# Kernel optimization log

Measured on AMD Instinct MI355X. Metric: run time of the kernel, lower is better.

## Reference

```python
import jax, jax.numpy as jnp
import numpy as np

IN_FEATS = 512
OUT_FEATS = 512


def _xavier(key, shape, gain):
    fan_in, fan_out = shape[1], shape[0]
    a = gain * np.sqrt(6.0 / (fan_in + fan_out))
    return jax.random.uniform(key, shape, jnp.float32, -a, a)


def setup_inputs() -> dict:
    key = jax.random.key(0)
    ks = jax.random.split(key, 8)
    num_dst, num_vir, num_src = 8192, 32768, 131072
    n_e0, n_e1 = 524288, 131072
    gain = np.sqrt(2.0)  # calculate_gain('relu')
    feat = jax.random.normal(ks[0], (num_dst + num_src, IN_FEATS), jnp.float32)
    W_self = _xavier(ks[1], (OUT_FEATS, IN_FEATS), gain)
    b_self = jnp.zeros((OUT_FEATS,), jnp.float32)
    W_neigh = _xavier(ks[2], (OUT_FEATS, IN_FEATS), gain)
    e0_src = jax.random.randint(ks[3], (n_e0,), 0, num_src, jnp.int64 if jax.config.jax_enable_x64 else jnp.int32)
    e0_dst = jax.random.randint(ks[4], (n_e0,), 0, num_vir, e0_src.dtype)
    e1_src = jax.random.randint(ks[5], (n_e1,), 0, num_vir, e0_src.dtype)
    e1_dst = jax.random.randint(ks[6], (n_e1,), 0, num_dst, e0_src.dtype)
    return {
        "feat": feat, "W_self": W_self, "b_self": b_self, "W_neigh": W_neigh,
        "e0_src": e0_src, "e0_dst": e0_dst, "e1_src": e1_src, "e1_dst": e1_dst,
        "num_dst": num_dst, "num_vir": num_vir,
    }


def _seg_mean(msgs, dst, n):
    # DGL fn.mean: mean over incoming edges; zero-in-degree nodes get 0.
    s = jax.ops.segment_sum(msgs, dst, num_segments=n)
    c = jax.ops.segment_sum(jnp.ones((dst.shape[0], 1), msgs.dtype), dst, num_segments=n)
    return s / jnp.maximum(c, 1.0)


def reference(feat, W_self, b_self, W_neigh, e0_src, e0_dst, e1_src, e1_dst, num_dst, num_vir):
    # feat_drop is identity (p=0.0)
    h_dst = feat[:num_dst] @ W_self.T + b_self              # [num_dst, out]
    feat_src = feat[num_dst:]                                # [num_src, in]
    h_src = feat_src @ W_neigh.T                             # [num_src, out]
    # block0: copy_u + mean -> virtual nodes
    h_vir = _seg_mean(h_src[e0_src], e0_dst, num_vir)        # [num_vir, out]
    # SPFeatureShuffle is identity in single-partition setting
    # block1: copy_u + mean -> dst nodes
    h_neigh = _seg_mean(h_vir[e1_src], e1_dst, num_dst)      # [num_dst, out]
    rst = h_dst + h_neigh                                    # activation=None, norm=None
    return rst
```

## Files before the change

### kernel.cpp

```cpp
#include <hip/hip_runtime.h>
#include <stdint.h>

#define NUM_DST 8192
#define NUM_VIR 32768
#define NUM_SRC 131072
#define F       512
#define CAP     64

typedef short bf16x8 __attribute__((ext_vector_type(8)));
typedef float f32x4  __attribute__((ext_vector_type(4)));
typedef float f32x2  __attribute__((ext_vector_type(2)));
typedef unsigned int u32x4 __attribute__((ext_vector_type(4)));

__device__ __forceinline__ unsigned short f2bf(float f) {
  union { float f; unsigned int u; } v; v.f = f;
  unsigned int u = v.u;
  unsigned int r = (u + 0x7fffu + ((u >> 16) & 1u)) >> 16;
  return (unsigned short)r;
}
__device__ __forceinline__ unsigned int pack2(float a, float b) {
  return (unsigned int)f2bf(a) | ((unsigned int)f2bf(b) << 16);
}

__global__ void prep_all(const int* __restrict__ e0s, const int* __restrict__ e0d, int ne0,
                         const int* __restrict__ e1s, const int* __restrict__ e1d, int ne1,
                         int* __restrict__ c0, int* __restrict__ b0,
                         int* __restrict__ c1, int* __restrict__ b1,
                         const float* __restrict__ feat,
                         const float* __restrict__ Wself, const float* __restrict__ Wneigh,
                         u32x4* __restrict__ a1, u32x4* __restrict__ fsrc8,
                         unsigned short* __restrict__ wcat,
                         int bktBlocks, int a1Blocks, int srcBlocks) {
  int b = blockIdx.x, t = threadIdx.x;
  if (b < bktBlocks) {
    int i = b * 256 + t;
    if (i < ne0) {
      int d = e0d[i];
      int r = atomicAdd(&c0[d], 1);
      if (r < CAP) b0[d * CAP + r] = e0s[i];
    } else {
      int j = i - ne0;
      if (j < ne1) {
        int d = e1d[j];
        int r = atomicAdd(&c1[d], 1);
        if (r < CAP) b1[d * CAP + r] = e1s[j];
      }
    }
  } else if (b < bktBlocks + a1Blocks) {
    size_t tid = (size_t)(b - bktBlocks) * 256 + t;
    const f32x4* fp = (const f32x4*)feat;
    f32x4 v0 = __builtin_nontemporal_load(&fp[tid * 2]);
    f32x4 v1 = __builtin_nontemporal_load(&fp[tid * 2 + 1]);
    u32x4 o;
    o.x = pack2(v0.x, v0.y); o.y = pack2(v0.z, v0.w);
    o.z = pack2(v1.x, v1.y); o.w = pack2(v1.z, v1.w);
    a1[tid] = o;
  } else if (b < bktBlocks + a1Blocks + srcBlocks) {
    size_t idx = (size_t)(b - bktBlocks - a1Blocks) * 256 + t;
    const f32x4* fp = (const f32x4*)(feat + (size_t)NUM_DST * F);
    f32x4 v0 = __builtin_nontemporal_load(&fp[idx * 4]);
    f32x4 v1 = __builtin_nontemporal_load(&fp[idx * 4 + 1]);
    f32x4 v2 = __builtin_nontemporal_load(&fp[idx * 4 + 2]);
    f32x4 v3 = __builtin_nontemporal_load(&fp[idx * 4 + 3]);
    u32x4 o;
    o.x = __builtin_amdgcn_cvt_pk_fp8_f32(v0.x, v0.y, 0u, 0);
    o.x = __builtin_amdgcn_cvt_pk_fp8_f32(v0.z, v0.w, o.x, 1);
    o.y = __builtin_amdgcn_cvt_pk_fp8_f32(v1.x, v1.y, 0u, 0);
    o.y = __builtin_amdgcn_cvt_pk_fp8_f32(v1.z, v1.w, o.y, 1);
    o.z = __builtin_amdgcn_cvt_pk_fp8_f32(v2.x, v2.y, 0u, 0);
    o.z = __builtin_amdgcn_cvt_pk_fp8_f32(v2.z, v2.w, o.z, 1);
    o.w = __builtin_amdgcn_cvt_pk_fp8_f32(v3.x, v3.y, 0u, 0);
    o.w = __builtin_amdgcn_cvt_pk_fp8_f32(v3.z, v3.w, o.w, 1);
    fsrc8[idx] = o;
  } else {
    int idx = (b - bktBlocks - a1Blocks - srcBlocks) * 256 + t;
    int n = idx >> 7, kb = (idx & 127) * 8;
    const float* src = (kb < F) ? (Wself + (size_t)n * F + kb)
                                : (Wneigh + (size_t)n * F + (kb - F));
    f32x4 v0 = __builtin_nontemporal_load((const f32x4*)src);
    f32x4 v1 = __builtin_nontemporal_load((const f32x4*)(src + 4));
    u32x4 o;
    o.x = pack2(v0.x, v0.y); o.y = pack2(v0.z, v0.w);
    o.z = pack2(v1.x, v1.y); o.w = pack2(v1.z, v1.w);
    *(u32x4*)(wcat + (size_t)n * 1024 + kb) = o;
  }
}

template<bool OUT_FP8>
__global__ void agg_gather(const uint4* __restrict__ tab, const int* __restrict__ cnt,
                           const int* __restrict__ bucket, void* __restrict__ outp) {
  int seg  = blockIdx.x * 4 + (threadIdx.x >> 6);
  int lane = threadIdx.x & 63;
  int half = lane >> 5;
  int l32  = lane & 31;
  int c = cnt[seg]; if (c > CAP) c = CAP;
  const int* bk = bucket + (size_t)seg * CAP;
  float a[16];
#pragma unroll
  for (int j = 0; j < 16; ++j) a[j] = 0.f;
  for (int i = half; i < c; i += 2) {
    int s = bk[i];
    uint4 u = tab[(size_t)s * 32 + l32];
    f32x2 p;
    p = __builtin_amdgcn_cvt_pk_f32_fp8(u.x, 0); a[0]  += p.x; a[1]  += p.y;
    p = __builtin_amdgcn_cvt_pk_f32_fp8(u.x, 1); a[2]  += p.x; a[3]  += p.y;
    p = __builtin_amdgcn_cvt_pk_f32_fp8(u.y, 0); a[4]  += p.x; a[5]  += p.y;
    p = __builtin_amdgcn_cvt_pk_f32_fp8(u.y, 1); a[6]  += p.x; a[7]  += p.y;
    p = __builtin_amdgcn_cvt_pk_f32_fp8(u.z, 0); a[8]  += p.x; a[9]  += p.y;
    p = __builtin_amdgcn_cvt_pk_f32_fp8(u.z, 1); a[10] += p.x; a[11] += p.y;
    p = __builtin_amdgcn_cvt_pk_f32_fp8(u.w, 0); a[12] += p.x; a[13] += p.y;
    p = __builtin_amdgcn_cvt_pk_f32_fp8(u.w, 1); a[14] += p.x; a[15] += p.y;
  }
#pragma unroll
  for (int j = 0; j < 16; ++j) a[j] += __shfl_xor(a[j], 32);
  float inv = 1.0f / (float)(c < 1 ? 1 : c);
  if (half == 0) {
    if (OUT_FP8) {
      uint4 o;
      o.x = __builtin_amdgcn_cvt_pk_fp8_f32(a[0] * inv,  a[1] * inv,  0u, 0);
      o.x = __builtin_amdgcn_cvt_pk_fp8_f32(a[2] * inv,  a[3] * inv,  o.x, 1);
      o.y = __builtin_amdgcn_cvt_pk_fp8_f32(a[4] * inv,  a[5] * inv,  0u, 0);
      o.y = __builtin_amdgcn_cvt_pk_fp8_f32(a[6] * inv,  a[7] * inv,  o.y, 1);
      o.z = __builtin_amdgcn_cvt_pk_fp8_f32(a[8] * inv,  a[9] * inv,  0u, 0);
      o.z = __builtin_amdgcn_cvt_pk_fp8_f32(a[10] * inv, a[11] * inv, o.z, 1);
      o.w = __builtin_amdgcn_cvt_pk_fp8_f32(a[12] * inv, a[13] * inv, 0u, 0);
      o.w = __builtin_amdgcn_cvt_pk_fp8_f32(a[14] * inv, a[15] * inv, o.w, 1);
      ((uint4*)outp)[(size_t)seg * 32 + l32] = o;
    } else {
      uint4 o0, o1;
      o0.x = pack2(a[0] * inv,  a[1] * inv);  o0.y = pack2(a[2] * inv,  a[3] * inv);
      o0.z = pack2(a[4] * inv,  a[5] * inv);  o0.w = pack2(a[6] * inv,  a[7] * inv);
      o1.x = pack2(a[8] * inv,  a[9] * inv);  o1.y = pack2(a[10] * inv, a[11] * inv);
      o1.z = pack2(a[12] * inv, a[13] * inv); o1.w = pack2(a[14] * inv, a[15] * inv);
      uint4* orow = (uint4*)outp + (size_t)seg * 64 + l32 * 2;
      orow[0] = o0;
      orow[1] = o1;
    }
  }
}

__global__ __launch_bounds__(256) void gemm_kernel(
    const unsigned short* __restrict__ A1, const unsigned short* __restrict__ A2,
    const unsigned short* __restrict__ W, const float* __restrict__ bias,
    float* __restrict__ out) {
  __shared__ unsigned short As[128 * 72];
  __shared__ unsigned short Bs[64 * 72];
  int t = threadIdx.x;
  int lane = t & 63, wid = t >> 6;
  int wm = wid & 1, wn = wid >> 1;
  int l16 = lane & 15, quad = lane >> 4;
  int m0 = blockIdx.x * 128, n0 = blockIdx.y * 64;

  f32x4 acc[4][2];
  for (int fi = 0; fi < 4; ++fi)
    for (int ni = 0; ni < 2; ++ni)
      acc[fi][ni] = (f32x4){0.f, 0.f, 0.f, 0.f};

  for (int kt = 0; kt < 16; ++kt) {
    const unsigned short* Asrc = (kt < 8) ? A1 : A2;
    int kk0 = (kt & 7) * 64;
#pragma unroll
    for (int r = 0; r < 4; ++r) {
      int q = r * 256 + t;
      int row = q >> 3, c = q & 7;
      uint4 v = *(const uint4*)(Asrc + (size_t)(m0 + row) * F + kk0 + c * 8);
      *(uint4*)(&As[row * 72 + c * 8]) = v;
    }
#pragma unroll
    for (int r = 0; r < 2; ++r) {
      int q = r * 256 + t;
      int row = q >> 3, c = q & 7;
      uint4 v = *(const uint4*)(W + (size_t)(n0 + row) * 1024 + kt * 64 + c * 8);
      *(uint4*)(&Bs[row * 72 + c * 8]) = v;
    }
    __syncthreads();
#pragma unroll
    for (int kk = 0; kk < 2; ++kk) {
      bf16x8 a[4], b[2];
#pragma unroll
      for (int fi = 0; fi < 4; ++fi)
        a[fi] = *(const bf16x8*)(&As[(wm * 64 + fi * 16 + l16) * 72 + kk * 32 + quad * 8]);
#pragma unroll
      for (int ni = 0; ni < 2; ++ni)
        b[ni] = *(const bf16x8*)(&Bs[(wn * 32 + ni * 16 + l16) * 72 + kk * 32 + quad * 8]);
#pragma unroll
      for (int fi = 0; fi < 4; ++fi)
#pragma unroll
        for (int ni = 0; ni < 2; ++ni)
          acc[fi][ni] = __builtin_amdgcn_mfma_f32_16x16x32_bf16(a[fi], b[ni], acc[fi][ni], 0, 0, 0);
    }
    __syncthreads();
  }
#pragma unroll
  for (int ni = 0; ni < 2; ++ni) {
    int n = n0 + wn * 32 + ni * 16 + l16;
    float bv = bias[n];
#pragma unroll
    for (int fi = 0; fi < 4; ++fi) {
#pragma unroll
      for (int reg = 0; reg < 4; ++reg) {
        int m = m0 + wm * 64 + fi * 16 + quad * 4 + reg;
        __builtin_nontemporal_store(acc[fi][ni][reg] + bv, &out[(size_t)m * F + n]);
      }
    }
  }
}

extern "C" void kernel_launch(void* const* d_in, const int* in_sizes, int n_in,
                              void* d_out, int out_size, void* d_ws, size_t ws_size,
                              hipStream_t stream) {
  const float* feat    = (const float*)d_in[0];
  const float* W_self  = (const float*)d_in[1];
  const float* b_self  = (const float*)d_in[2];
  const float* W_neigh = (const float*)d_in[3];
  const int*   e0_src  = (const int*)d_in[4];
  const int*   e0_dst  = (const int*)d_in[5];
  const int*   e1_src  = (const int*)d_in[6];
  const int*   e1_dst  = (const int*)d_in[7];
  int ne0 = in_sizes[4];
  int ne1 = in_sizes[6];

  char* ws = (char*)d_ws;
  size_t off = 0;
  auto nxt = [&](size_t bytes) -> char* {
    char* p = ws + off;
    off += (bytes + 255) & ~(size_t)255;
    return p;
  };
  int* cnt0    = (int*)nxt((size_t)NUM_VIR * 4);
  int* cnt1    = (int*)nxt((size_t)NUM_DST * 4);
  int* bucket0 = (int*)nxt((size_t)NUM_VIR * CAP * 4);
  int* bucket1 = (int*)nxt((size_t)NUM_DST * CAP * 4);
  u32x4* fsrc8 = (u32x4*)nxt((size_t)NUM_SRC * F);
  u32x4* a1    = (u32x4*)nxt((size_t)NUM_DST * F * 2);
  uint2* fvir8 = (uint2*)nxt((size_t)NUM_VIR * F);
  uint4* a2    = (uint4*)nxt((size_t)NUM_DST * F * 2);
  unsigned short* wcat = (unsigned short*)nxt((size_t)F * 1024 * 2);
  (void)ws_size;

  hipMemsetAsync(cnt0, 0, (size_t)(NUM_VIR + NUM_DST) * 4, stream);

  int neTot     = ne0 + ne1;
  int bktBlocks = (neTot + 255) / 256;
  int a1Blocks  = NUM_DST * F / 8 / 256;
  int srcBlocks = NUM_SRC * F / 16 / 256;
  prep_all<<<bktBlocks + a1Blocks + srcBlocks + 256, 256, 0, stream>>>(
      e0_src, e0_dst, ne0, e1_src, e1_dst, ne1,
      cnt0, bucket0, cnt1, bucket1,
      feat, W_self, W_neigh, a1, fsrc8, wcat,
      bktBlocks, a1Blocks, srcBlocks);

  agg_gather<true><<<NUM_VIR / 4, 256, 0, stream>>>((const uint4*)fsrc8, cnt0, bucket0, fvir8);
  agg_gather<false><<<NUM_DST / 4, 256, 0, stream>>>((const uint4*)fvir8, cnt1, bucket1, a2);

  dim3 ggrid(NUM_DST / 128, F / 64);
  gemm_kernel<<<ggrid, 256, 0, stream>>>((const unsigned short*)a1, (const unsigned short*)a2,
                                         wcat, b_self, (float*)d_out);
}
```

Baseline: 520.9 us.

## Gather four edge rows per wave in aggregation and XOR-swizzle GEMM LDS tiles

```diff
diff --git a/kernel.cpp b/kernel.cpp
--- a/kernel.cpp
+++ b/kernel.cpp
@@ -91,50 +91,85 @@
                            const int* __restrict__ bucket, void* __restrict__ outp) {
   int seg  = blockIdx.x * 4 + (threadIdx.x >> 6);
   int lane = threadIdx.x & 63;
-  int half = lane >> 5;
-  int l32  = lane & 31;
+  int q    = lane >> 4;
+  int l16  = lane & 15;
   int c = cnt[seg]; if (c > CAP) c = CAP;
   const int* bk = bucket + (size_t)seg * CAP;
-  float a[16];
-#pragma unroll
-  for (int j = 0; j < 16; ++j) a[j] = 0.f;
-  for (int i = half; i < c; i += 2) {
-    int s = bk[i];
-    uint4 u = tab[(size_t)s * 32 + l32];
+  int myidx = bk[lane];
+  const uint4* lanebase = tab + l16 * 2;
+  float a[32];
+#pragma unroll
+  for (int j = 0; j < 32; ++j) a[j] = 0.f;
+  int nit = (c + 3) >> 2;
+  for (int k = 0; k < nit; ++k) {
+    int i = k * 4 + q;
+    bool ok = i < c;
+    int s = __shfl(myidx, i);
+    uint4 u0 = make_uint4(0u, 0u, 0u, 0u);
+    uint4 u1 = make_uint4(0u, 0u, 0u, 0u);
+    if (ok) {
+      const uint4* rp = lanebase + (size_t)s * 32;
+      u0 = rp[0];
+      u1 = rp[1];
+    }
     f32x2 p;
-    p = __builtin_amdgcn_cvt_pk_f32_fp8(u.x, 0); a[0]  += p.x; a[1]  += p.y;
-    p = __builtin_amdgcn_cvt_pk_f32_fp8(u.x, 1); a[2]  += p.x; a[3]  += p.y;
-    p = __builtin_amdgcn_cvt_pk_f32_fp8(u.y, 0); a[4]  += p.x; a[5]  += p.y;
-    p = __builtin_amdgcn_cvt_pk_f32_fp8(u.y, 1); a[6]  += p.x; a[7]  += p.y;
-    p = __builtin_amdgcn_cvt_pk_f32_fp8(u.z, 0); a[8]  += p.x; a[9]  += p.y;
-    p = __builtin_amdgcn_cvt_pk_f32_fp8(u.z, 1); a[10] += p.x; a[11] += p.y;
-    p = __builtin_amdgcn_cvt_pk_f32_fp8(u.w, 0); a[12] += p.x; a[13] += p.y;
-    p = __builtin_amdgcn_cvt_pk_f32_fp8(u.w, 1); a[14] += p.x; a[15] += p.y;
-  }
-#pragma unroll
-  for (int j = 0; j < 16; ++j) a[j] += __shfl_xor(a[j], 32);
+    p = __builtin_amdgcn_cvt_pk_f32_fp8(u0.x, 0); a[0]  += p.x; a[1]  += p.y;
+    p = __builtin_amdgcn_cvt_pk_f32_fp8(u0.x, 1); a[2]  += p.x; a[3]  += p.y;
+    p = __builtin_amdgcn_cvt_pk_f32_fp8(u0.y, 0); a[4]  += p.x; a[5]  += p.y;
+    p = __builtin_amdgcn_cvt_pk_f32_fp8(u0.y, 1); a[6]  += p.x; a[7]  += p.y;
+    p = __builtin_amdgcn_cvt_pk_f32_fp8(u0.z, 0); a[8]  += p.x; a[9]  += p.y;
+    p = __builtin_amdgcn_cvt_pk_f32_fp8(u0.z, 1); a[10] += p.x; a[11] += p.y;
+    p = __builtin_amdgcn_cvt_pk_f32_fp8(u0.w, 0); a[12] += p.x; a[13] += p.y;
+    p = __builtin_amdgcn_cvt_pk_f32_fp8(u0.w, 1); a[14] += p.x; a[15] += p.y;
+    p = __builtin_amdgcn_cvt_pk_f32_fp8(u1.x, 0); a[16] += p.x; a[17] += p.y;
+    p = __builtin_amdgcn_cvt_pk_f32_fp8(u1.x, 1); a[18] += p.x; a[19] += p.y;
+    p = __builtin_amdgcn_cvt_pk_f32_fp8(u1.y, 0); a[20] += p.x; a[21] += p.y;
+    p = __builtin_amdgcn_cvt_pk_f32_fp8(u1.y, 1); a[22] += p.x; a[23] += p.y;
+    p = __builtin_amdgcn_cvt_pk_f32_fp8(u1.z, 0); a[24] += p.x; a[25] += p.y;
+    p = __builtin_amdgcn_cvt_pk_f32_fp8(u1.z, 1); a[26] += p.x; a[27] += p.y;
+    p = __builtin_amdgcn_cvt_pk_f32_fp8(u1.w, 0); a[28] += p.x; a[29] += p.y;
+    p = __builtin_amdgcn_cvt_pk_f32_fp8(u1.w, 1); a[30] += p.x; a[31] += p.y;
+  }
+#pragma unroll
+  for (int j = 0; j < 32; ++j) {
+    a[j] += __shfl_xor(a[j], 16);
+    a[j] += __shfl_xor(a[j], 32);
+  }
   float inv = 1.0f / (float)(c < 1 ? 1 : c);
-  if (half == 0) {
+  if (q == 0) {
     if (OUT_FP8) {
-      uint4 o;
-      o.x = __builtin_amdgcn_cvt_pk_fp8_f32(a[0] * inv,  a[1] * inv,  0u, 0);
-      o.x = __builtin_amdgcn_cvt_pk_fp8_f32(a[2] * inv,  a[3] * inv,  o.x, 1);
-      o.y = __builtin_amdgcn_cvt_pk_fp8_f32(a[4] * inv,  a[5] * inv,  0u, 0);
-      o.y = __builtin_amdgcn_cvt_pk_fp8_f32(a[6] * inv,  a[7] * inv,  o.y, 1);
-      o.z = __builtin_amdgcn_cvt_pk_fp8_f32(a[8] * inv,  a[9] * inv,  0u, 0);
-      o.z = __builtin_amdgcn_cvt_pk_fp8_f32(a[10] * inv, a[11] * inv, o.z, 1);
-      o.w = __builtin_amdgcn_cvt_pk_fp8_f32(a[12] * inv, a[13] * inv, 0u, 0);
-      o.w = __builtin_amdgcn_cvt_pk_fp8_f32(a[14] * inv, a[15] * inv, o.w, 1);
-      ((uint4*)outp)[(size_t)seg * 32 + l32] = o;
+      uint4 o0, o1;
+      o0.x = __builtin_amdgcn_cvt_pk_fp8_f32(a[0] * inv,  a[1] * inv,  0u, 0);
+      o0.x = __builtin_amdgcn_cvt_pk_fp8_f32(a[2] * inv,  a[3] * inv,  o0.x, 1);
+      o0.y = __builtin_amdgcn_cvt_pk_fp8_f32(a[4] * inv,  a[5] * inv,  0u, 0);
+      o0.y = __builtin_amdgcn_cvt_pk_fp8_f32(a[6] * inv,  a[7] * inv,  o0.y, 1);
+      o0.z = __builtin_amdgcn_cvt_pk_fp8_f32(a[8] * inv,  a[9] * inv,  0u, 0);
+      o0.z = __builtin_amdgcn_cvt_pk_fp8_f32(a[10] * inv, a[11] * inv, o0.z, 1);
+      o0.w = __builtin_amdgcn_cvt_pk_fp8_f32(a[12] * inv, a[13] * inv, 0u, 0);
+      o0.w = __builtin_amdgcn_cvt_pk_fp8_f32(a[14] * inv, a[15] * inv, o0.w, 1);
+      o1.x = __builtin_amdgcn_cvt_pk_fp8_f32(a[16] * inv, a[17] * inv, 0u, 0);
+      o1.x = __builtin_amdgcn_cvt_pk_fp8_f32(a[18] * inv, a[19] * inv, o1.x, 1);
+      o1.y = __builtin_amdgcn_cvt_pk_fp8_f32(a[20] * inv, a[21] * inv, 0u, 0);
+      o1.y = __builtin_amdgcn_cvt_pk_fp8_f32(a[22] * inv, a[23] * inv, o1.y, 1);
+      o1.z = __builtin_amdgcn_cvt_pk_fp8_f32(a[24] * inv, a[25] * inv, 0u, 0);
+      o1.z = __builtin_amdgcn_cvt_pk_fp8_f32(a[26] * inv, a[27] * inv, o1.z, 1);
+      o1.w = __builtin_amdgcn_cvt_pk_fp8_f32(a[28] * inv, a[29] * inv, 0u, 0);
+      o1.w = __builtin_amdgcn_cvt_pk_fp8_f32(a[30] * inv, a[31] * inv, o1.w, 1);
+      uint4* op = (uint4*)outp + (size_t)seg * 32 + l16 * 2;
+      op[0] = o0;
+      op[1] = o1;
     } else {
-      uint4 o0, o1;
-      o0.x = pack2(a[0] * inv,  a[1] * inv);  o0.y = pack2(a[2] * inv,  a[3] * inv);
-      o0.z = pack2(a[4] * inv,  a[5] * inv);  o0.w = pack2(a[6] * inv,  a[7] * inv);
-      o1.x = pack2(a[8] * inv,  a[9] * inv);  o1.y = pack2(a[10] * inv, a[11] * inv);
+      uint4 o0, o1, o2, o3;
+      o0.x = pack2(a[0]  * inv, a[1]  * inv); o0.y = pack2(a[2]  * inv, a[3]  * inv);
+      o0.z = pack2(a[4]  * inv, a[5]  * inv); o0.w = pack2(a[6]  * inv, a[7]  * inv);
+      o1.x = pack2(a[8]  * inv, a[9]  * inv); o1.y = pack2(a[10] * inv, a[11] * inv);
       o1.z = pack2(a[12] * inv, a[13] * inv); o1.w = pack2(a[14] * inv, a[15] * inv);
-      uint4* orow = (uint4*)outp + (size_t)seg * 64 + l32 * 2;
-      orow[0] = o0;
-      orow[1] = o1;
+      o2.x = pack2(a[16] * inv, a[17] * inv); o2.y = pack2(a[18] * inv, a[19] * inv);
+      o2.z = pack2(a[20] * inv, a[21] * inv); o2.w = pack2(a[22] * inv, a[23] * inv);
+      o3.x = pack2(a[24] * inv, a[25] * inv); o3.y = pack2(a[26] * inv, a[27] * inv);
+      o3.z = pack2(a[28] * inv, a[29] * inv); o3.w = pack2(a[30] * inv, a[31] * inv);
+      uint4* op = (uint4*)outp + (size_t)seg * 64 + l16 * 4;
+      op[0] = o0; op[1] = o1; op[2] = o2; op[3] = o3;
     }
   }
 }
@@ -143,8 +178,8 @@
     const unsigned short* __restrict__ A1, const unsigned short* __restrict__ A2,
     const unsigned short* __restrict__ W, const float* __restrict__ bias,
     float* __restrict__ out) {
-  __shared__ unsigned short As[128 * 72];
-  __shared__ unsigned short Bs[64 * 72];
+  __shared__ unsigned short As[128 * 64];
+  __shared__ unsigned short Bs[64 * 64];
   int t = threadIdx.x;
   int lane = t & 63, wid = t >> 6;
   int wm = wid & 1, wn = wid >> 1;
@@ -161,28 +196,34 @@
     int kk0 = (kt & 7) * 64;
 #pragma unroll
     for (int r = 0; r < 4; ++r) {
-      int q = r * 256 + t;
-      int row = q >> 3, c = q & 7;
-      uint4 v = *(const uint4*)(Asrc + (size_t)(m0 + row) * F + kk0 + c * 8);
-      *(uint4*)(&As[row * 72 + c * 8]) = v;
+      int qq = r * 256 + t;
+      int row = qq >> 3, cc = qq & 7;
+      uint4 v = *(const uint4*)(Asrc + (size_t)(m0 + row) * F + kk0 + cc * 8);
+      *(uint4*)(&As[row * 64 + ((cc ^ (row & 7)) * 8)]) = v;
     }
 #pragma unroll
     for (int r = 0; r < 2; ++r) {
-      int q = r * 256 + t;
-      int row = q >> 3, c = q & 7;
-      uint4 v = *(const uint4*)(W + (size_t)(n0 + row) * 1024 + kt * 64 + c * 8);
-      *(uint4*)(&Bs[row * 72 + c * 8]) = v;
+      int qq = r * 256 + t;
+      int row = qq >> 3, cc = qq & 7;
+      uint4 v = *(const uint4*)(W + (size_t)(n0 + row) * 1024 + kt * 64 + cc * 8);
+      *(uint4*)(&Bs[row * 64 + ((cc ^ (row & 7)) * 8)]) = v;
     }
     __syncthreads();
 #pragma unroll
     for (int kk = 0; kk < 2; ++kk) {
       bf16x8 a[4], b[2];
 #pragma unroll
-      for (int fi = 0; fi < 4; ++fi)
-        a[fi] = *(const bf16x8*)(&As[(wm * 64 + fi * 16 + l16) * 72 + kk * 32 + quad * 8]);
-#pragma unroll
-      for (int ni = 0; ni < 2; ++ni)
-        b[ni] = *(const bf16x8*)(&Bs[(wn * 32 + ni * 16 + l16) * 72 + kk * 32 + quad * 8]);
+      for (int fi = 0; fi < 4; ++fi) {
+        int row = wm * 64 + fi * 16 + l16;
+        int ch = (kk * 4 + quad) ^ (row & 7);
+        a[fi] = *(const bf16x8*)(&As[row * 64 + ch * 8]);
+      }
+#pragma unroll
+      for (int ni = 0; ni < 2; ++ni) {
+        int row = wn * 32 + ni * 16 + l16;
+        int ch = (kk * 4 + quad) ^ (row & 7);
+        b[ni] = *(const bf16x8*)(&Bs[row * 64 + ch * 8]);
+      }
 #pragma unroll
       for (int fi = 0; fi < 4; ++fi)
 #pragma unroll
```

Measured after the change: 524.2 us. Within noise of the previous version (+0.6%).
